# Performance work log

Measured on AMD Instinct MI355X. Metric: run time of the kernel, lower is better.

## Reference

```python
import jax, jax.numpy as jnp
import numpy as np

B, S, HID = 2, 2048, 768
NH, HD = 12, 64  # num heads, head dim


def setup_inputs() -> dict:
    key = jax.random.key(0)
    ks = jax.random.split(key, 10)
    scale = 0.02
    return {
        "hidden_states": jax.random.normal(ks[0], (B, S, HID), jnp.float32),
        "rel_pos": jax.random.normal(ks[1], (B, NH, S, S), jnp.float32),
        "rel_2d_pos": jax.random.normal(ks[2], (B, NH, S, S), jnp.float32),
        "attention_mask": jax.random.randint(ks[3], (B, 1, S, S), 0, 2, jnp.int32),
        "Wq": jax.random.normal(ks[4], (HID, HID), jnp.float32) * scale,
        "bq": jnp.zeros((HID,), jnp.float32),
        "Wk": jax.random.normal(ks[5], (HID, HID), jnp.float32) * scale,
        "bk": jnp.zeros((HID,), jnp.float32),
        "Wv": jax.random.normal(ks[6], (HID, HID), jnp.float32) * scale,
        "bv": jnp.zeros((HID,), jnp.float32),
    }


def _heads(x):
    # [B,S,HID] -> [B,NH,S,HD]
    return x.reshape(B, S, NH, HD).transpose(0, 2, 1, 3)


def reference(hidden_states, rel_pos, rel_2d_pos, attention_mask, Wq, bq, Wk, bk, Wv, bv):
    q = _heads(hidden_states @ Wq.T + bq) / jnp.sqrt(jnp.asarray(HD, hidden_states.dtype))
    k = _heads(hidden_states @ Wk.T + bk)
    v = _heads(hidden_states @ Wv.T + bv)
    scores = jnp.einsum('bhsd,bhtd->bhst', q, k)
    scores = scores + rel_pos + rel_2d_pos
    scores = jnp.where(attention_mask.astype(bool), jnp.finfo(jnp.float32).min, scores.astype(jnp.float32))
    probs = jax.nn.softmax(scores, axis=-1).astype(v.dtype)
    ctx = jnp.einsum('bhst,bhtd->bhsd', probs, v)
    return ctx.transpose(0, 2, 1, 3).reshape(B, S, HID)
```

## Files before the change

### kernel.cpp

```cpp
#include <hip/hip_runtime.h>

#define B_ 2
#define S_ 2048
#define HID_ 768
#define NH_ 12
#define HD_ 64

typedef unsigned short u16;
typedef __attribute__((ext_vector_type(8))) short bf16x8;
typedef __attribute__((ext_vector_type(4))) float f32x4;

static __device__ inline u16 f2bf(float f) {
    union { float f; unsigned u; } v; v.f = f;
    unsigned r = v.u + 0x7fffu + ((v.u >> 16) & 1u);
    return (u16)(r >> 16);
}

#define LDS_BARRIER() asm volatile("s_waitcnt lgkmcnt(0)\n\ts_barrier" ::: "memory")

__global__ void cast_bf16(const float* __restrict__ src, u16* __restrict__ dst, int n) {
    int i = (blockIdx.x * blockDim.x + threadIdx.x) * 4;
    if (i < n) {
        float4 v = *(const float4*)(src + i);
        unsigned lo = (unsigned)f2bf(v.x) | ((unsigned)f2bf(v.y) << 16);
        unsigned hi = (unsigned)f2bf(v.z) | ((unsigned)f2bf(v.w) << 16);
        uint2 o; o.x = lo; o.y = hi;
        *(uint2*)(dst + i) = o;
    }
}

__global__ __launch_bounds__(256) void qkv_gemm(
    const u16* __restrict__ hsb, const u16* __restrict__ wcat,
    const float* __restrict__ bq, const float* __restrict__ bk, const float* __restrict__ bv,
    u16* __restrict__ Qg, u16* __restrict__ Kg, u16* __restrict__ Vtg)
{
    __shared__ u16 As[64 * 40];
    __shared__ u16 Bs[64 * 40];
    __shared__ u16 Vs[64 * 72];

    const int m0 = blockIdx.x * 64;
    const int n0 = blockIdx.y * 64;
    const int tid = threadIdx.x;
    const int wave = tid >> 6, lane = tid & 63;
    const int l = lane & 15, quad = lane >> 4;

    f32x4 acc[4];
#pragma unroll
    for (int t = 0; t < 4; t++) acc[t] = (f32x4){0.f, 0.f, 0.f, 0.f};

    const int srow = tid >> 2;
    const int skg = (tid & 3) * 8;

    for (int k0 = 0; k0 < HID_; k0 += 32) {
        *(int4*)(&As[srow * 40 + skg]) = *(const int4*)(&hsb[(size_t)(m0 + srow) * HID_ + k0 + skg]);
        *(int4*)(&Bs[srow * 40 + skg]) = *(const int4*)(&wcat[(size_t)(n0 + srow) * HID_ + k0 + skg]);
        __syncthreads();
        bf16x8 a = *(const bf16x8*)(&As[(wave * 16 + l) * 40 + quad * 8]);
#pragma unroll
        for (int t = 0; t < 4; t++) {
            bf16x8 b = *(const bf16x8*)(&Bs[(t * 16 + l) * 40 + quad * 8]);
            acc[t] = __builtin_amdgcn_mfma_f32_16x16x32_bf16(a, b, acc[t], 0, 0, 0);
        }
        __syncthreads();
    }

    const int proj = n0 / HID_;
    const int cbase = n0 - proj * HID_;
    const int h = cbase >> 6;
    const int bidx = m0 >> 11;
    const int srow0 = m0 & (S_ - 1);
    const float* bias = (proj == 0) ? bq : ((proj == 1) ? bk : bv);

    if (proj < 2) {
        u16* dst = (proj == 0) ? Qg : Kg;
        const float sc = (proj == 0) ? 0.125f : 1.0f;
#pragma unroll
        for (int t = 0; t < 4; t++) {
            const int d = t * 16 + l;
            const float bb = bias[cbase + d];
#pragma unroll
            for (int rr = 0; rr < 4; rr++) {
                int s = srow0 + wave * 16 + quad * 4 + rr;
                float v = (acc[t][rr] + bb) * sc;
                dst[(((size_t)bidx * NH_ + h) * S_ + s) * HD_ + d] = f2bf(v);
            }
        }
    } else {
#pragma unroll
        for (int t = 0; t < 4; t++) {
            const int d = t * 16 + l;
            const float bb = bias[cbase + d];
#pragma unroll
            for (int rr = 0; rr < 4; rr++) {
                int sl = wave * 16 + quad * 4 + rr;
                Vs[d * 72 + sl] = f2bf(acc[t][rr] + bb);
            }
        }
        __syncthreads();
        const int drow = tid >> 2;
        const int sseg = (tid & 3) * 16;
        size_t base = (((size_t)bidx * NH_ + h) * HD_ + drow) * S_ + srow0 + sseg;
        *(int4*)(&Vtg[base])     = *(const int4*)(&Vs[drow * 72 + sseg]);
        *(int4*)(&Vtg[base + 8]) = *(const int4*)(&Vs[drow * 72 + sseg + 8]);
    }
}

__global__ __launch_bounds__(256) void attn(
    const u16* __restrict__ Qg, const u16* __restrict__ Kg, const u16* __restrict__ Vtg,
    const float* __restrict__ rel, const float* __restrict__ rel2,
    const int* __restrict__ mask, float* __restrict__ out)
{
    __shared__ u16 Ks[64 * 72];
    __shared__ u16 Vts[64 * 72];
    __shared__ u16 Ps[4 * 16 * 72];

    const int q0 = blockIdx.x * 64;
    const int h = blockIdx.y;
    const int b = blockIdx.z;
    const int tid = threadIdx.x;
    const int wave = tid >> 6, lane = tid & 63;
    const int l = lane & 15, quad = lane >> 4;
    const int bh = b * NH_ + h;

    const float NEG = -3.4028234663852886e38f;

    bf16x8 qf[2];
    {
        const int qr = q0 + wave * 16 + l;
        qf[0] = *(const bf16x8*)(&Qg[((size_t)bh * S_ + qr) * HD_ + quad * 8]);
        qf[1] = *(const bf16x8*)(&Qg[((size_t)bh * S_ + qr) * HD_ + 32 + quad * 8]);
    }

    f32x4 o[4];
#pragma unroll
    for (int t = 0; t < 4; t++) o[t] = (f32x4){0.f, 0.f, 0.f, 0.f};
    float m_run = NEG, l_run = 0.f;

    const int srow = tid >> 2;
    const int sseg = (tid & 3) * 8;

    const int qrow = q0 + wave * 16 + l;
    const float* relR  = rel  + (size_t)bh * S_ * S_ + (size_t)qrow * S_;
    const float* rel2R = rel2 + (size_t)bh * S_ * S_ + (size_t)qrow * S_;
    const int*   maskR = mask + (size_t)b * S_ * S_ + (size_t)qrow * S_;

    float4 pr1[4], pr2[4];
    int4 pmk[4];
#pragma unroll
    for (int t = 0; t < 4; t++) {
        const int c = t * 16 + quad * 4;
        pr1[t] = *(const float4*)(relR + c);
        pr2[t] = *(const float4*)(rel2R + c);
        pmk[t] = *(const int4*)(maskR + c);
    }

    for (int k0 = 0; k0 < S_; k0 += 64) {
        size_t kg = ((size_t)bh * S_ + k0 + srow) * HD_;
        int4 ka = *(const int4*)(&Kg[kg + sseg]);
        int4 kb = *(const int4*)(&Kg[kg + 32 + sseg]);
        size_t vg = ((size_t)bh * HD_ + srow) * S_ + k0;
        int4 va = *(const int4*)(&Vtg[vg + sseg]);
        int4 vb = *(const int4*)(&Vtg[vg + 32 + sseg]);

        f32x4 sacc[4];
#pragma unroll
        for (int t = 0; t < 4; t++) {
            sacc[t][0] = pmk[t].x ? NEG : pr1[t].x + pr2[t].x;
            sacc[t][1] = pmk[t].y ? NEG : pr1[t].y + pr2[t].y;
            sacc[t][2] = pmk[t].z ? NEG : pr1[t].z + pr2[t].z;
            sacc[t][3] = pmk[t].w ? NEG : pr1[t].w + pr2[t].w;
        }

        if (k0 + 64 < S_) {
#pragma unroll
            for (int t = 0; t < 4; t++) {
                const int c = k0 + 64 + t * 16 + quad * 4;
                pr1[t] = *(const float4*)(relR + c);
                pr2[t] = *(const float4*)(rel2R + c);
                pmk[t] = *(const int4*)(maskR + c);
            }
        }

        *(int4*)(&Ks[srow * 72 + sseg])       = ka;
        *(int4*)(&Ks[srow * 72 + 32 + sseg])  = kb;
        *(int4*)(&Vts[srow * 72 + sseg])      = va;
        *(int4*)(&Vts[srow * 72 + 32 + sseg]) = vb;
        LDS_BARRIER();

#pragma unroll
        for (int t = 0; t < 4; t++) {
            bf16x8 b0 = *(const bf16x8*)(&Ks[(t * 16 + l) * 72 + quad * 8]);
            sacc[t] = __builtin_amdgcn_mfma_f32_16x16x32_bf16(b0, qf[0], sacc[t], 0, 0, 0);
            bf16x8 b1 = *(const bf16x8*)(&Ks[(t * 16 + l) * 72 + 32 + quad * 8]);
            sacc[t] = __builtin_amdgcn_mfma_f32_16x16x32_bf16(b1, qf[1], sacc[t], 0, 0, 0);
        }

        float mx = NEG;
#pragma unroll
        for (int t = 0; t < 4; t++)
#pragma unroll
            for (int rr = 0; rr < 4; rr++) mx = fmaxf(mx, sacc[t][rr]);
        mx = fmaxf(mx, __shfl_xor(mx, 16, 64));
        mx = fmaxf(mx, __shfl_xor(mx, 32, 64));
        float mnew = fmaxf(m_run, mx);
        float alpha = __expf(m_run - mnew);
        float rs = 0.f;
#pragma unroll
        for (int t = 0; t < 4; t++)
#pragma unroll
            for (int rr = 0; rr < 4; rr++) {
                float p = __expf(sacc[t][rr] - mnew);
                sacc[t][rr] = p;
                rs += p;
            }
        rs += __shfl_xor(rs, 16, 64);
        rs += __shfl_xor(rs, 32, 64);
        l_run = l_run * alpha + rs;
        m_run = mnew;

        float av[4];
#pragma unroll
        for (int rr = 0; rr < 4; rr++) av[rr] = __shfl(alpha, quad * 4 + rr, 64);
#pragma unroll
        for (int dt = 0; dt < 4; dt++)
#pragma unroll
            for (int rr = 0; rr < 4; rr++) o[dt][rr] *= av[rr];

#pragma unroll
        for (int t = 0; t < 4; t++) {
            unsigned p01 = (unsigned)f2bf(sacc[t][0]) | ((unsigned)f2bf(sacc[t][1]) << 16);
            unsigned p23 = (unsigned)f2bf(sacc[t][2]) | ((unsigned)f2bf(sacc[t][3]) << 16);
            uint2 pw; pw.x = p01; pw.y = p23;
            *(uint2*)(&Ps[(wave * 16 + l) * 72 + t * 16 + quad * 4]) = pw;
        }

        bf16x8 pa0 = *(const bf16x8*)(&Ps[(wave * 16 + l) * 72 + quad * 8]);
        bf16x8 pa1 = *(const bf16x8*)(&Ps[(wave * 16 + l) * 72 + 32 + quad * 8]);
#pragma unroll
        for (int dt = 0; dt < 4; dt++) {
            bf16x8 v0 = *(const bf16x8*)(&Vts[(dt * 16 + l) * 72 + quad * 8]);
            o[dt] = __builtin_amdgcn_mfma_f32_16x16x32_bf16(pa0, v0, o[dt], 0, 0, 0);
            bf16x8 v1 = *(const bf16x8*)(&Vts[(dt * 16 + l) * 72 + 32 + quad * 8]);
            o[dt] = __builtin_amdgcn_mfma_f32_16x16x32_bf16(pa1, v1, o[dt], 0, 0, 0);
        }
        LDS_BARRIER();
    }

    float lv[4];
#pragma unroll
    for (int rr = 0; rr < 4; rr++) lv[rr] = __shfl(l_run, quad * 4 + rr, 64);
#pragma unroll
    for (int dt = 0; dt < 4; dt++) {
#pragma unroll
        for (int rr = 0; rr < 4; rr++) {
            const int row = q0 + wave * 16 + quad * 4 + rr;
            out[((size_t)b * S_ + row) * HID_ + h * HD_ + dt * 16 + l] = o[dt][rr] / lv[rr];
        }
    }
}

extern "C" void kernel_launch(void* const* d_in, const int* in_sizes, int n_in,
                              void* d_out, int out_size, void* d_ws, size_t ws_size,
                              hipStream_t stream) {
    const float* hs   = (const float*)d_in[0];
    const float* rel  = (const float*)d_in[1];
    const float* rel2 = (const float*)d_in[2];
    const int*   mask = (const int*)d_in[3];
    const float* Wq = (const float*)d_in[4];
    const float* bq = (const float*)d_in[5];
    const float* Wk = (const float*)d_in[6];
    const float* bk = (const float*)d_in[7];
    const float* Wv = (const float*)d_in[8];
    const float* bv = (const float*)d_in[9];
    float* out = (float*)d_out;

    char* ws = (char*)d_ws;
    u16* hsb  = (u16*)(ws);
    u16* wcat = (u16*)(ws + 6291456);
    u16* Qg   = (u16*)(ws + 9830400);
    u16* Kg   = (u16*)(ws + 16121856);
    u16* Vtg  = (u16*)(ws + 22413312);

    cast_bf16<<<3072, 256, 0, stream>>>(hs, hsb, B_ * S_ * HID_);
    cast_bf16<<<576, 256, 0, stream>>>(Wq, wcat,             HID_ * HID_);
    cast_bf16<<<576, 256, 0, stream>>>(Wk, wcat + HID_ * HID_,     HID_ * HID_);
    cast_bf16<<<576, 256, 0, stream>>>(Wv, wcat + 2 * HID_ * HID_, HID_ * HID_);

    qkv_gemm<<<dim3(64, 36), 256, 0, stream>>>(hsb, wcat, bq, bk, bv, Qg, Kg, Vtg);

    attn<<<dim3(S_ / 64, NH_, B_), 256, 0, stream>>>(Qg, Kg, Vtg, rel, rel2, mask, out);
}
```

Measured before the change: 900.0 us.

## Split attention key range across two blocks and merge with combine kernel

The attention grid is split along the key dimension into two halves (flash-decoding style). Each block writes unnormalized partial outputs plus its running max and sum to workspace, and a new combine kernel merges them with log-sum-exp rescaling. This doubles the block count from 768 to 1536 for better CU occupancy and latency hiding. A launch-bounds occupancy hint was added. The cost is extra global traffic for the partials and one more kernel launch.

```diff
diff --git a/kernel.cpp b/kernel.cpp
--- a/kernel.cpp
+++ b/kernel.cpp
@@ -5,6 +5,9 @@
 #define HID_ 768
 #define NH_ 12
 #define HD_ 64
+#define NSPLIT 2
+#define KSPAN (S_ / NSPLIT)
+#define NROWS (B_ * NH_ * S_)
 
 typedef unsigned short u16;
 typedef __attribute__((ext_vector_type(8))) short bf16x8;
@@ -105,10 +108,11 @@
     }
 }
 
-__global__ __launch_bounds__(256) void attn(
+__global__ __launch_bounds__(256, 5) void attn(
     const u16* __restrict__ Qg, const u16* __restrict__ Kg, const u16* __restrict__ Vtg,
     const float* __restrict__ rel, const float* __restrict__ rel2,
-    const int* __restrict__ mask, float* __restrict__ out)
+    const int* __restrict__ mask,
+    float* __restrict__ Opart, float* __restrict__ Mpart, float* __restrict__ Lpart)
 {
     __shared__ u16 Ks[64 * 72];
     __shared__ u16 Vts[64 * 72];
@@ -116,11 +120,14 @@
 
     const int q0 = blockIdx.x * 64;
     const int h = blockIdx.y;
-    const int b = blockIdx.z;
+    const int b = blockIdx.z / NSPLIT;
+    const int split = blockIdx.z - b * NSPLIT;
     const int tid = threadIdx.x;
     const int wave = tid >> 6, lane = tid & 63;
     const int l = lane & 15, quad = lane >> 4;
     const int bh = b * NH_ + h;
+    const int kbase = split * KSPAN;
+    const int kend = kbase + KSPAN;
 
     const float NEG = -3.4028234663852886e38f;
 
@@ -148,13 +155,13 @@
     int4 pmk[4];
 #pragma unroll
     for (int t = 0; t < 4; t++) {
-        const int c = t * 16 + quad * 4;
+        const int c = kbase + t * 16 + quad * 4;
         pr1[t] = *(const float4*)(relR + c);
         pr2[t] = *(const float4*)(rel2R + c);
         pmk[t] = *(const int4*)(maskR + c);
     }
 
-    for (int k0 = 0; k0 < S_; k0 += 64) {
+    for (int k0 = kbase; k0 < kend; k0 += 64) {
         size_t kg = ((size_t)bh * S_ + k0 + srow) * HD_;
         int4 ka = *(const int4*)(&Kg[kg + sseg]);
         int4 kb = *(const int4*)(&Kg[kg + 32 + sseg]);
@@ -171,7 +178,7 @@
             sacc[t][3] = pmk[t].w ? NEG : pr1[t].w + pr2[t].w;
         }
 
-        if (k0 + 64 < S_) {
+        if (k0 + 64 < kend) {
 #pragma unroll
             for (int t = 0; t < 4; t++) {
                 const int c = k0 + 64 + t * 16 + quad * 4;
@@ -246,17 +253,46 @@
         LDS_BARRIER();
     }
 
-    float lv[4];
-#pragma unroll
-    for (int rr = 0; rr < 4; rr++) lv[rr] = __shfl(l_run, quad * 4 + rr, 64);
+    float* Op = Opart + (((size_t)split * B_ * NH_ + bh) * S_ + q0) * HD_;
 #pragma unroll
     for (int dt = 0; dt < 4; dt++) {
 #pragma unroll
         for (int rr = 0; rr < 4; rr++) {
-            const int row = q0 + wave * 16 + quad * 4 + rr;
-            out[((size_t)b * S_ + row) * HID_ + h * HD_ + dt * 16 + l] = o[dt][rr] / lv[rr];
-        }
-    }
+            const int row = wave * 16 + quad * 4 + rr;
+            Op[(size_t)row * HD_ + dt * 16 + l] = o[dt][rr];
+        }
+    }
+    if (quad == 0) {
+        const size_t mi = ((size_t)split * B_ * NH_ + bh) * S_ + q0 + wave * 16 + l;
+        Mpart[mi] = m_run;
+        Lpart[mi] = l_run;
+    }
+}
+
+__global__ __launch_bounds__(256) void combine(
+    const float* __restrict__ Op, const float* __restrict__ Mp, const float* __restrict__ Lp,
+    float* __restrict__ out)
+{
+    const int idx = blockIdx.x * 256 + threadIdx.x;
+    const int r = idx >> 4;
+    const int dseg = (idx & 15) * 4;
+    const float m0 = Mp[r], m1 = Mp[NROWS + r];
+    const float l0 = Lp[r], l1 = Lp[NROWS + r];
+    const float m = fmaxf(m0, m1);
+    const float a0 = __expf(m0 - m), a1 = __expf(m1 - m);
+    const float inv = 1.0f / (l0 * a0 + l1 * a1);
+    const float4 o0 = *(const float4*)(Op + (size_t)r * HD_ + dseg);
+    const float4 o1 = *(const float4*)(Op + ((size_t)NROWS + r) * HD_ + dseg);
+    float4 res;
+    res.x = (o0.x * a0 + o1.x * a1) * inv;
+    res.y = (o0.y * a0 + o1.y * a1) * inv;
+    res.z = (o0.z * a0 + o1.z * a1) * inv;
+    res.w = (o0.w * a0 + o1.w * a1) * inv;
+    const int bh_ = r >> 11;
+    const int s = r & (S_ - 1);
+    const int b = bh_ / NH_;
+    const int h = bh_ - b * NH_;
+    *(float4*)(out + ((size_t)(b * S_ + s)) * HID_ + h * HD_ + dseg) = res;
 }
 
 extern "C" void kernel_launch(void* const* d_in, const int* in_sizes, int n_in,
@@ -275,11 +311,14 @@
     float* out = (float*)d_out;
 
     char* ws = (char*)d_ws;
-    u16* hsb  = (u16*)(ws);
-    u16* wcat = (u16*)(ws + 6291456);
-    u16* Qg   = (u16*)(ws + 9830400);
-    u16* Kg   = (u16*)(ws + 16121856);
-    u16* Vtg  = (u16*)(ws + 22413312);
+    u16* hsb   = (u16*)(ws);
+    u16* wcat  = (u16*)(ws + 6291456);
+    u16* Qg    = (u16*)(ws + 9830400);
+    u16* Kg    = (u16*)(ws + 16121856);
+    u16* Vtg   = (u16*)(ws + 22413312);
+    float* Opart = (float*)(ws + 28704768);
+    float* Mpart = (float*)(ws + 53870592);
+    float* Lpart = (float*)(ws + 54263808);
 
     cast_bf16<<<3072, 256, 0, stream>>>(hs, hsb, B_ * S_ * HID_);
     cast_bf16<<<576, 256, 0, stream>>>(Wq, wcat,             HID_ * HID_);
@@ -288,5 +327,8 @@
 
     qkv_gemm<<<dim3(64, 36), 256, 0, stream>>>(hsb, wcat, bq, bk, bv, Qg, Kg, Vtg);
 
-    attn<<<dim3(S_ / 64, NH_, B_), 256, 0, stream>>>(Qg, Kg, Vtg, rel, rel2, mask, out);
-}
+    attn<<<dim3(S_ / 64, NH_, B_ * NSPLIT), 256, 0, stream>>>(
+        Qg, Kg, Vtg, rel, rel2, mask, Opart, Mpart, Lpart);
+
+    combine<<<(NROWS * 16) / 256, 256, 0, stream>>>(Opart, Mpart, Lpart, out);
+}
```

Result: slower. 1.698 ms (+88.7%).
